# Kernel optimization log

Measured on AMD Instinct MI355X. Metric: run time of the kernel, lower is better.

The kernel has to match this reference:

```python
import jax, jax.numpy as jnp
import numpy as np
import math

B, L, D, H = 8, 1024, 1024, 16  # batch, seq, hidden_dim, num_heads
HD = D // H  # head dim = 64
CLUSTERING = True  # softmax over query axis (dim 1 of [B*H, Lq, Lk])


def setup_inputs() -> dict:
    key = jax.random.key(0)
    ks = jax.random.split(key, 12)
    s = 1.0 / math.sqrt(D)  # torch Linear default init scale-ish
    return {
        "x_q": jax.random.normal(ks[0], (B, L, D), jnp.float32),
        "x_k": jax.random.normal(ks[1], (B, L, D), jnp.float32),
        "x_v": jax.random.normal(ks[2], (B, L, D), jnp.float32),
        "mask": jnp.ones((B, L), dtype=bool),
        "Wq": jax.random.uniform(ks[3], (D, D), jnp.float32, -s, s),
        "bq": jax.random.uniform(ks[4], (D,), jnp.float32, -s, s),
        "Wk": jax.random.uniform(ks[5], (D, D), jnp.float32, -s, s),
        "bk": jax.random.uniform(ks[6], (D,), jnp.float32, -s, s),
        "Wv": jax.random.uniform(ks[7], (D, D), jnp.float32, -s, s),
        "bv": jax.random.uniform(ks[8], (D,), jnp.float32, -s, s),
        "Wo": jax.random.uniform(ks[9], (D, D), jnp.float32, -s, s),
        "bo": jax.random.uniform(ks[10], (D,), jnp.float32, -s, s),
    }


def reference(x_q, x_k, x_v, mask, Wq, bq, Wk, bk, Wv, bv, Wo, bo):
    # Projections (weights stored [in, out])
    Q = x_q @ Wq + bq  # [B, Lq, D]
    K = x_k @ Wk + bk  # [B, Lk, D]
    V = x_v @ Wv + bv  # [B, Lk, D]
    b, lq, _ = Q.shape
    lk = K.shape[1]
    # torch.cat(split(dim_split, 2), dim=0) == reshape to [B, L, H, HD] heads
    Qh = Q.reshape(b, lq, H, HD)
    Kh = K.reshape(b, lk, H, HD)
    Vh = V.reshape(b, lk, H, HD)
    # Scores scaled by sqrt(hidden_dim), NOT sqrt(head_dim) (faithful to source)
    scores = jnp.einsum("bqhd,bkhd->bhqk", Qh, Kh) / math.sqrt(D)
    # NOTE: source computes inf_mask but never applies it -> mask unused.
    if CLUSTERING:
        A = jax.nn.softmax(scores, axis=2)  # softmax over QUERY axis
    else:
        A = jax.nn.softmax(scores, axis=3)  # standard: over key axis
    # dropout ratio 0.0 -> identity
    out = jnp.einsum("bhqk,bkhd->bqhd", A, Vh).reshape(b, lq, D)
    return out @ Wo + bo
```

## Files before the change

### kernel.cpp

```cpp
#include <hip/hip_runtime.h>
#include <hip/hip_bf16.h>

#define B_ 8
#define L_ 1024
#define D_ 1024
#define H_ 16
#define HD_ 64

typedef short short8 __attribute__((ext_vector_type(8)));
typedef float floatx4 __attribute__((ext_vector_type(4)));
typedef unsigned short u16;

__device__ __forceinline__ u16 f2bf(float f) {
  union { float f; unsigned u; } v; v.f = f;
  unsigned r = v.u + 0x7fffu + ((v.u >> 16) & 1u);
  return (u16)(r >> 16);
}
__device__ __forceinline__ unsigned pk2(float a, float b) {
  union { float f; unsigned u; } x, y; x.f = a; y.f = b;
  return __builtin_amdgcn_perm(y.u + 0x8000u, x.u + 0x8000u, 0x07060302u);
}
__device__ __forceinline__ floatx4 mfma16(short8 a, short8 b, floatx4 c) {
  return __builtin_amdgcn_mfma_f32_16x16x32_bf16(a, b, c, 0, 0, 0);
}
__device__ __forceinline__ void gl2lds16(const void* g, void* l) {
  __builtin_amdgcn_global_load_lds(
      (const __attribute__((address_space(1))) void*)g,
      (__attribute__((address_space(3))) void*)l, 16, 0, 0);
}

__global__ __launch_bounds__(256) void cvtx_k(const float* __restrict__ x,
                                              u16* __restrict__ y) {
  size_t i = ((size_t)blockIdx.x * 256 + threadIdx.x) * 8;
  float4 a = *(const float4*)(x + i);
  float4 b = *(const float4*)(x + i + 4);
  uint4 u = make_uint4(pk2(a.x, a.y), pk2(a.z, a.w), pk2(b.x, b.y), pk2(b.z, b.w));
  *(uint4*)(y + i) = u;
}

__global__ __launch_bounds__(256) void cvtw_k(const float* __restrict__ W,
                                              u16* __restrict__ Wt) {
  const int kt = blockIdx.x, nt = blockIdx.y;
  __shared__ __align__(16) u16 t[64 * 72];
  const int tid = threadIdx.x;
  #pragma unroll
  for (int i = 0; i < 4; ++i) {
    int idx = i * 256 + tid;
    int r = idx >> 4, c4 = idx & 15;
    float4 v = *(const float4*)(W + (size_t)(kt * 64 + r) * 1024 + nt * 64 + c4 * 4);
    t[(c4 * 4 + 0) * 72 + r] = f2bf(v.x);
    t[(c4 * 4 + 1) * 72 + r] = f2bf(v.y);
    t[(c4 * 4 + 2) * 72 + r] = f2bf(v.z);
    t[(c4 * 4 + 3) * 72 + r] = f2bf(v.w);
  }
  __syncthreads();
  #pragma unroll
  for (int i = 0; i < 2; ++i) {
    int idx = i * 256 + tid;
    int n = idx >> 3, k8 = idx & 7;
    short8 v = *(const short8*)(&t[n * 72 + k8 * 8]);
    *(short8*)(Wt + (size_t)(nt * 64 + n) * 1024 + kt * 64 + k8 * 8) = v;
  }
}

template<int AMODE, int OUTM>
__global__ __launch_bounds__(256, 2) void gemm2_k(const void* __restrict__ Ap,
    const u16* __restrict__ Bt, const float* __restrict__ bias,
    void* __restrict__ Cp, const float* __restrict__ inv)
{
  const int nt = blockIdx.x, mt = blockIdx.y;
  const int tid = threadIdx.x, lane = tid & 63, w = tid >> 6;
  const int quad = lane >> 4, l16 = lane & 15;
  const int wm = w >> 1, wn = w & 1;
  const int m0 = mt * 128, n0 = nt * 128;

  constexpr int ABYTES = AMODE ? 8192 : 16384;
  constexpr int STG = ABYTES + 8192;
  constexpr int SBYTES = (OUTM == 2 && STG < 34816) ? 34816 : STG;
  __shared__ __align__(16) char smem[SBYTES];
  char* AsB = smem;
  char* BsB = smem + ABYTES;

  const floatx4 fz = {0.f, 0.f, 0.f, 0.f};
  floatx4 acc[4][4];
  #pragma unroll
  for (int i = 0; i < 4; ++i)
    #pragma unroll
    for (int j = 0; j < 4; ++j) acc[i][j] = fz;

  const int sw4 = (l16 & 3) ^ ((l16 >> 2) & 3);

  for (int k0 = 0; k0 < 1024; k0 += 32) {
    #pragma unroll
    for (int seg = 0; seg < 2; ++seg) {
      int cI = seg * 256 + w * 64 + lane;
      int n = cI >> 2, sl = cI & 3;
      int kc = sl ^ ((n & 3) ^ ((n >> 2) & 3));
      gl2lds16(Bt + (size_t)(n0 + n) * 1024 + k0 + kc * 8, BsB + cI * 16);
    }
    if constexpr (AMODE == 0) {
      const float* A = (const float*)Ap;
      #pragma unroll
      for (int seg = 0; seg < 4; ++seg) {
        int cI = seg * 256 + w * 64 + lane;
        int r = cI >> 3, sl = cI & 7;
        int kc = sl ^ ((r & 7) ^ ((r >> 3) & 7));
        gl2lds16(A + (size_t)(m0 + r) * 1024 + k0 + kc * 4, AsB + cI * 16);
      }
    } else {
      const u16* A = (const u16*)Ap;
      #pragma unroll
      for (int seg = 0; seg < 2; ++seg) {
        int cI = seg * 256 + w * 64 + lane;
        int r = cI >> 2, sl = cI & 3;
        int kc = sl ^ ((r & 3) ^ ((r >> 2) & 3));
        gl2lds16(A + (size_t)(m0 + r) * 1024 + k0 + kc * 8, AsB + cI * 16);
      }
    }
    __syncthreads();

    short8 af[4], bfv[4];
    #pragma unroll
    for (int mf = 0; mf < 4; ++mf) {
      int row = wm * 64 + mf * 16 + l16;
      if constexpr (AMODE == 0) {
        int s0 = (quad * 2) ^ (l16 & 7) ^ ((mf * 2 + (l16 >> 3)) & 7);
        float4 x0 = *(const float4*)(AsB + row * 128 + s0 * 16);
        float4 x1 = *(const float4*)(AsB + row * 128 + (s0 ^ 1) * 16);
        union { uint4 u; short8 s; } uu;
        uu.u = make_uint4(pk2(x0.x, x0.y), pk2(x0.z, x0.w),
                          pk2(x1.x, x1.y), pk2(x1.z, x1.w));
        af[mf] = uu.s;
      } else {
        af[mf] = *(const short8*)(AsB + row * 64 + (quad ^ sw4) * 16);
      }
    }
    #pragma unroll
    for (int nf = 0; nf < 4; ++nf) {
      int row = wn * 64 + nf * 16 + l16;
      bfv[nf] = *(const short8*)(BsB + row * 64 + (quad ^ sw4) * 16);
    }
    #pragma unroll
    for (int mf = 0; mf < 4; ++mf)
      #pragma unroll
      for (int nf = 0; nf < 4; ++nf)
        acc[mf][nf] = mfma16(af[mf], bfv[nf], acc[mf][nf]);
    __syncthreads();
  }

  float bv[4];
  #pragma unroll
  for (int nf = 0; nf < 4; ++nf) bv[nf] = bias[n0 + wn * 64 + nf * 16 + l16];

  if constexpr (OUTM == 0) {
    float* C = (float*)Cp;
    #pragma unroll
    for (int mf = 0; mf < 4; ++mf)
      #pragma unroll
      for (int nf = 0; nf < 4; ++nf) {
        int n = n0 + wn * 64 + nf * 16 + l16;
        #pragma unroll
        for (int r = 0; r < 4; ++r) {
          int m = m0 + wm * 64 + mf * 16 + quad * 4 + r;
          C[(size_t)m * 1024 + n] = acc[mf][nf][r] + bv[nf];
        }
      }
  } else if constexpr (OUTM == 1) {
    u16* C = (u16*)Cp;
    #pragma unroll
    for (int mf = 0; mf < 4; ++mf)
      #pragma unroll
      for (int nf = 0; nf < 4; ++nf) {
        int n = n0 + wn * 64 + nf * 16 + l16;
        #pragma unroll
        for (int r = 0; r < 4; ++r) {
          int m = m0 + wm * 64 + mf * 16 + quad * 4 + r;
          int bb = m >> 10, l = m & 1023, hh = n >> 6, hd = n & 63;
          C[((size_t)((bb * H_ + hh) * L_) + l) * HD_ + hd] =
              f2bf(acc[mf][nf][r] + bv[nf]);
        }
      }
  } else {
    u16* ct = (u16*)smem;
    const int bb = m0 >> 10;
    const int hrow = bb * 16 + (n0 >> 6) + wn;
    float ivv[4][4];
    #pragma unroll
    for (int mf = 0; mf < 4; ++mf)
      #pragma unroll
      for (int r = 0; r < 4; ++r)
        ivv[mf][r] = inv[(size_t)hrow * 1024 + (m0 & 1023) + wm * 64 + mf * 16 + quad * 4 + r];
    #pragma unroll
    for (int mf = 0; mf < 4; ++mf)
      #pragma unroll
      for (int nf = 0; nf < 4; ++nf)
        #pragma unroll
        for (int r = 0; r < 4; ++r) {
          float val = (acc[mf][nf][r] + bv[nf]) * ivv[mf][r];
          ct[(wn * 64 + nf * 16 + l16) * 136 + wm * 64 + mf * 16 + quad * 4 + r] = f2bf(val);
        }
    __syncthreads();
    u16* Vt = (u16*)Cp;
    #pragma unroll
    for (int i = 0; i < 8; ++i) {
      int cc = i * 256 + tid;
      int n = cc >> 4, l8 = cc & 15;
      int g = l8 >> 2, q2 = l8 & 3;
      int mloc = g * 32 + q2 * 4;
      uint2 lo = *(const uint2*)(&ct[n * 136 + mloc]);
      uint2 hi = *(const uint2*)(&ct[n * 136 + mloc + 16]);
      uint4 uv = make_uint4(lo.x, lo.y, hi.x, hi.y);
      *(uint4*)(Vt + ((size_t)bb * 1024 + n0 + n) * 1024 + (m0 & 1023) + l8 * 8) = uv;
    }
  }
}

__global__ __launch_bounds__(256, 2) void colsum2_k(const u16* __restrict__ Q,
    const u16* __restrict__ K, float* __restrict__ inv)
{
  const int ktb = blockIdx.x, h = blockIdx.y, b = blockIdx.z;
  const int tid = threadIdx.x, lane = tid & 63, w = tid >> 6;
  const int quad = lane >> 4, l16 = lane & 15;
  const size_t hb = (size_t)(b * H_ + h) * L_ * HD_;
  const u16* Qh = Q + hb;
  const u16* Kh = K + hb;
  const int kbase = ktb * 256 + w * 64;
  const floatx4 fz = {0.f, 0.f, 0.f, 0.f};
  const float cexp = 0.04508422f;

  __shared__ __align__(16) u16 qsm[8192];

  short8 kf[4][2];
  #pragma unroll
  for (int nf = 0; nf < 4; ++nf)
    #pragma unroll
    for (int ks = 0; ks < 2; ++ks)
      kf[nf][ks] = *(const short8*)(Kh + (size_t)(kbase + nf * 16 + l16) * 64 + ks * 32 + quad * 8);

  float cs[4] = {0.f, 0.f, 0.f, 0.f};
  for (int qc = 0; qc < 8; ++qc) {
    #pragma unroll
    for (int seg = 0; seg < 4; ++seg) {
      int cI = seg * 256 + w * 64 + lane;
      int row = cI >> 3, sl = cI & 7;
      gl2lds16(Qh + (size_t)(qc * 128 + row) * 64 + ((sl ^ (row & 7)) * 8), (char*)qsm + cI * 16);
    }
    __syncthreads();
    #pragma unroll
    for (int mf = 0; mf < 8; ++mf) {
      short8 qf0 = *(const short8*)(&qsm[(mf * 16 + l16) * 64 + ((quad ^ (l16 & 7)) * 8)]);
      short8 qf1 = *(const short8*)(&qsm[(mf * 16 + l16) * 64 + (((4 + quad) ^ (l16 & 7)) * 8)]);
      floatx4 sacc[4];
      #pragma unroll
      for (int nf = 0; nf < 4; ++nf) {
        floatx4 s = mfma16(qf0, kf[nf][0], fz);
        sacc[nf] = mfma16(qf1, kf[nf][1], s);
      }
      #pragma unroll
      for (int nf = 0; nf < 4; ++nf)
        #pragma unroll
        for (int r = 0; r < 4; ++r)
          cs[nf] += __builtin_amdgcn_exp2f(sacc[nf][r] * cexp);
    }
    __syncthreads();
  }
  #pragma unroll
  for (int nf = 0; nf < 4; ++nf) {
    cs[nf] += __shfl_xor(cs[nf], 16);
    cs[nf] += __shfl_xor(cs[nf], 32);
  }
  if (quad == 0) {
    #pragma unroll
    for (int nf = 0; nf < 4; ++nf)
      inv[(size_t)(b * H_ + h) * L_ + kbase + nf * 16 + l16] = 1.0f / cs[nf];
  }
}

__global__ __launch_bounds__(256, 2) void attn3_k(const u16* __restrict__ Q,
    const u16* __restrict__ K, const u16* __restrict__ Vt, u16* __restrict__ O)
{
  const int qb = blockIdx.x, h = blockIdx.y, b = blockIdx.z;
  const int tid = threadIdx.x, lane = tid & 63, w = tid >> 6;
  const int quad = lane >> 4, l16 = lane & 15;
  const size_t hb = (size_t)(b * H_ + h) * L_ * HD_;
  const u16* Qh = Q + hb;
  const u16* Kh = K + hb;
  const u16* Vh = Vt + ((size_t)b * D_ + h * HD_) * L_;
  const int q0 = qb * 256 + w * 64;
  const floatx4 fz = {0.f, 0.f, 0.f, 0.f};
  const float cexp = 0.04508422f;

  __shared__ __align__(16) u16 smem[18432];
  u16* ksb = smem;
  u16* vsb = smem + 4096;

  short8 qf[4][2];
  #pragma unroll
  for (int qs = 0; qs < 4; ++qs)
    #pragma unroll
    for (int ks = 0; ks < 2; ++ks)
      qf[qs][ks] = *(const short8*)(Qh + (size_t)(q0 + qs * 16 + l16) * 64 + ks * 32 + quad * 8);

  floatx4 oT[4][4];
  #pragma unroll
  for (int i = 0; i < 4; ++i)
    #pragma unroll
    for (int j = 0; j < 4; ++j) oT[i][j] = fz;

  for (int kc = 0; kc < 16; ++kc) {
    const int kk = kc * 64;
    #pragma unroll
    for (int seg = 0; seg < 2; ++seg) {
      int cI = seg * 256 + w * 64 + lane;
      int row = cI >> 3, sl = cI & 7;
      gl2lds16(Kh + (size_t)(kk + row) * 64 + ((sl ^ (row & 7)) * 8), (char*)ksb + cI * 16);
    }
    #pragma unroll
    for (int seg = 0; seg < 2; ++seg) {
      int cI = seg * 256 + w * 64 + lane;
      int row = cI >> 3, sl = cI & 7;
      gl2lds16(Vh + (size_t)row * L_ + kk + ((sl ^ (row & 7)) * 8), (char*)vsb + cI * 16);
    }
    __syncthreads();

    short8 pt[2][4];
    #pragma unroll
    for (int p = 0; p < 2; ++p) {
      short8 ka0[2], ka1[2];
      #pragma unroll
      for (int ks = 0; ks < 2; ++ks) {
        ka0[ks] = *(const short8*)(&ksb[((2 * p) * 16 + l16) * 64 + (((ks * 4 + quad) ^ (l16 & 7)) * 8)]);
        ka1[ks] = *(const short8*)(&ksb[((2 * p + 1) * 16 + l16) * 64 + (((ks * 4 + quad) ^ (l16 & 7)) * 8)]);
      }
      #pragma unroll
      for (int qs = 0; qs < 4; ++qs) {
        floatx4 s0 = mfma16(ka0[0], qf[qs][0], fz);
        s0 = mfma16(ka0[1], qf[qs][1], s0);
        floatx4 s1 = mfma16(ka1[0], qf[qs][0], fz);
        s1 = mfma16(ka1[1], qf[qs][1], s1);
        float e0 = __builtin_amdgcn_exp2f(s0[0] * cexp);
        float e1 = __builtin_amdgcn_exp2f(s0[1] * cexp);
        float e2 = __builtin_amdgcn_exp2f(s0[2] * cexp);
        float e3 = __builtin_amdgcn_exp2f(s0[3] * cexp);
        float f0 = __builtin_amdgcn_exp2f(s1[0] * cexp);
        float f1 = __builtin_amdgcn_exp2f(s1[1] * cexp);
        float f2 = __builtin_amdgcn_exp2f(s1[2] * cexp);
        float f3 = __builtin_amdgcn_exp2f(s1[3] * cexp);
        union { uint4 u; short8 s; } pu;
        pu.u = make_uint4(pk2(e0, e1), pk2(e2, e3), pk2(f0, f1), pk2(f2, f3));
        pt[p][qs] = pu.s;
      }
    }
    #pragma unroll
    for (int p = 0; p < 2; ++p) {
      #pragma unroll
      for (int ds = 0; ds < 4; ++ds) {
        short8 va = *(const short8*)(&vsb[(ds * 16 + l16) * 64 + (((p * 4 + quad) ^ (l16 & 7)) * 8)]);
        #pragma unroll
        for (int qs = 0; qs < 4; ++qs)
          oT[ds][qs] = mfma16(va, pt[p][qs], oT[ds][qs]);
      }
    }
    __syncthreads();
  }

  u16* ot = smem + w * 4608;
  #pragma unroll
  for (int ds = 0; ds < 4; ++ds)
    #pragma unroll
    for (int qs = 0; qs < 4; ++qs)
      #pragma unroll
      for (int r = 0; r < 4; ++r)
        ot[(qs * 16 + l16) * 72 + ds * 16 + quad * 4 + r] = f2bf(oT[ds][qs][r]);
  __syncthreads();
  #pragma unroll
  for (int i = 0; i < 8; ++i) {
    int cc = i * 64 + lane;
    int ql = cc >> 3, d8 = cc & 7;
    short8 v = *(const short8*)(&ot[ql * 72 + d8 * 8]);
    *(short8*)(O + ((size_t)b * L_ + q0 + ql) * D_ + h * HD_ + d8 * 8) = v;
  }
}

extern "C" void kernel_launch(void* const* d_in, const int* in_sizes, int n_in,
                              void* d_out, int out_size, void* d_ws, size_t ws_size,
                              hipStream_t stream) {
  const float* xq = (const float*)d_in[0];
  const float* xk = (const float*)d_in[1];
  const float* xv = (const float*)d_in[2];
  const float* Wq = (const float*)d_in[4];
  const float* bq = (const float*)d_in[5];
  const float* Wk = (const float*)d_in[6];
  const float* bk = (const float*)d_in[7];
  const float* Wv = (const float*)d_in[8];
  const float* bv = (const float*)d_in[9];
  const float* Wo = (const float*)d_in[10];
  const float* bo = (const float*)d_in[11];

  char* ws = (char*)d_ws;
  const size_t MB16 = 16u << 20;
  u16* Xbf  = (u16*)(ws);
  u16* Vtb  = (u16*)(ws);
  u16* Qb   = (u16*)(ws + MB16);
  u16* WT2  = (u16*)(ws + MB16);
  u16* Kb   = (u16*)(ws + 2 * MB16);
  u16* WT   = (u16*)(ws + 3 * MB16);
  float* invb = (float*)(ws + 3 * MB16 + (2u << 20));
  u16* Ob   = (u16*)(ws + 3 * MB16);

  dim3 blk(256);
  dim3 gw(16, 16);
  dim3 gg(8, 64);

  cvtx_k<<<4096, blk, 0, stream>>>(xq, Xbf);
  cvtw_k<<<gw, blk, 0, stream>>>(Wq, WT);
  gemm2_k<1, 1><<<gg, blk, 0, stream>>>(Xbf, WT, bq, Qb, nullptr);

  cvtx_k<<<4096, blk, 0, stream>>>(xk, Xbf);
  cvtw_k<<<gw, blk, 0, stream>>>(Wk, WT);
  gemm2_k<1, 1><<<gg, blk, 0, stream>>>(Xbf, WT, bk, Kb, nullptr);

  colsum2_k<<<dim3(4, 16, 8), blk, 0, stream>>>(Qb, Kb, invb);

  cvtw_k<<<gw, blk, 0, stream>>>(Wv, WT);
  gemm2_k<0, 2><<<gg, blk, 0, stream>>>(xv, WT, bv, Vtb, invb);

  attn3_k<<<dim3(4, 16, 8), blk, 0, stream>>>(Qb, Kb, Vtb, Ob);

  cvtw_k<<<gw, blk, 0, stream>>>(Wo, WT2);
  gemm2_k<1, 0><<<gg, blk, 0, stream>>>(Ob, WT2, bo, (float*)d_out, nullptr);
}
```

Measured before the change: 373.4 us.

## Double K-step tiles in GEMM and attention, batch conversion kernels into fewer launches

```diff
diff --git a/kernel.cpp b/kernel.cpp
--- a/kernel.cpp
+++ b/kernel.cpp
@@ -29,8 +29,11 @@
       (__attribute__((address_space(3))) void*)l, 16, 0, 0);
 }
 
-__global__ __launch_bounds__(256) void cvtx_k(const float* __restrict__ x,
-                                              u16* __restrict__ y) {
+__global__ __launch_bounds__(256) void cvtx3_k(const float* __restrict__ x0,
+    const float* __restrict__ x1, const float* __restrict__ x2,
+    u16* __restrict__ y0, u16* __restrict__ y1, u16* __restrict__ y2) {
+  const float* x = blockIdx.y == 0 ? x0 : (blockIdx.y == 1 ? x1 : x2);
+  u16* y = blockIdx.y == 0 ? y0 : (blockIdx.y == 1 ? y1 : y2);
   size_t i = ((size_t)blockIdx.x * 256 + threadIdx.x) * 8;
   float4 a = *(const float4*)(x + i);
   float4 b = *(const float4*)(x + i + 4);
@@ -38,8 +41,14 @@
   *(uint4*)(y + i) = u;
 }
 
-__global__ __launch_bounds__(256) void cvtw_k(const float* __restrict__ W,
-                                              u16* __restrict__ Wt) {
+__global__ __launch_bounds__(256) void cvtw4_k(
+    const float* __restrict__ W0, const float* __restrict__ W1,
+    const float* __restrict__ W2, const float* __restrict__ W3,
+    u16* __restrict__ T0, u16* __restrict__ T1,
+    u16* __restrict__ T2, u16* __restrict__ T3) {
+  const int z = blockIdx.z;
+  const float* W = z == 0 ? W0 : (z == 1 ? W1 : (z == 2 ? W2 : W3));
+  u16* Wt = z == 0 ? T0 : (z == 1 ? T1 : (z == 2 ? T2 : T3));
   const int kt = blockIdx.x, nt = blockIdx.y;
   __shared__ __align__(16) u16 t[64 * 72];
   const int tid = threadIdx.x;
@@ -74,8 +83,8 @@
   const int wm = w >> 1, wn = w & 1;
   const int m0 = mt * 128, n0 = nt * 128;
 
-  constexpr int ABYTES = AMODE ? 8192 : 16384;
-  constexpr int STG = ABYTES + 8192;
+  constexpr int ABYTES = AMODE ? 16384 : 32768;
+  constexpr int STG = ABYTES + 16384;
   constexpr int SBYTES = (OUTM == 2 && STG < 34816) ? 34816 : STG;
   __shared__ __align__(16) char smem[SBYTES];
   char* AsB = smem;
@@ -88,63 +97,64 @@
     #pragma unroll
     for (int j = 0; j < 4; ++j) acc[i][j] = fz;
 
-  const int sw4 = (l16 & 3) ^ ((l16 >> 2) & 3);
-
-  for (int k0 = 0; k0 < 1024; k0 += 32) {
-    #pragma unroll
-    for (int seg = 0; seg < 2; ++seg) {
+  for (int k0 = 0; k0 < 1024; k0 += 64) {
+    #pragma unroll
+    for (int seg = 0; seg < 4; ++seg) {
       int cI = seg * 256 + w * 64 + lane;
-      int n = cI >> 2, sl = cI & 3;
-      int kc = sl ^ ((n & 3) ^ ((n >> 2) & 3));
-      gl2lds16(Bt + (size_t)(n0 + n) * 1024 + k0 + kc * 8, BsB + cI * 16);
+      int r = cI >> 3, sl = cI & 7;
+      int kc = sl ^ (r & 7);
+      gl2lds16(Bt + (size_t)(n0 + r) * 1024 + k0 + kc * 8, BsB + cI * 16);
     }
     if constexpr (AMODE == 0) {
       const float* A = (const float*)Ap;
+      #pragma unroll
+      for (int seg = 0; seg < 8; ++seg) {
+        int cI = seg * 256 + w * 64 + lane;
+        int r = cI >> 4, sl = cI & 15;
+        int kc = sl ^ (r & 15);
+        gl2lds16(A + (size_t)(m0 + r) * 1024 + k0 + kc * 4, AsB + cI * 16);
+      }
+    } else {
+      const u16* A = (const u16*)Ap;
       #pragma unroll
       for (int seg = 0; seg < 4; ++seg) {
         int cI = seg * 256 + w * 64 + lane;
         int r = cI >> 3, sl = cI & 7;
-        int kc = sl ^ ((r & 7) ^ ((r >> 3) & 7));
-        gl2lds16(A + (size_t)(m0 + r) * 1024 + k0 + kc * 4, AsB + cI * 16);
-      }
-    } else {
-      const u16* A = (const u16*)Ap;
-      #pragma unroll
-      for (int seg = 0; seg < 2; ++seg) {
-        int cI = seg * 256 + w * 64 + lane;
-        int r = cI >> 2, sl = cI & 3;
-        int kc = sl ^ ((r & 3) ^ ((r >> 2) & 3));
+        int kc = sl ^ (r & 7);
         gl2lds16(A + (size_t)(m0 + r) * 1024 + k0 + kc * 8, AsB + cI * 16);
       }
     }
     __syncthreads();
 
-    short8 af[4], bfv[4];
-    #pragma unroll
-    for (int mf = 0; mf < 4; ++mf) {
-      int row = wm * 64 + mf * 16 + l16;
-      if constexpr (AMODE == 0) {
-        int s0 = (quad * 2) ^ (l16 & 7) ^ ((mf * 2 + (l16 >> 3)) & 7);
-        float4 x0 = *(const float4*)(AsB + row * 128 + s0 * 16);
-        float4 x1 = *(const float4*)(AsB + row * 128 + (s0 ^ 1) * 16);
-        union { uint4 u; short8 s; } uu;
-        uu.u = make_uint4(pk2(x0.x, x0.y), pk2(x0.z, x0.w),
-                          pk2(x1.x, x1.y), pk2(x1.z, x1.w));
-        af[mf] = uu.s;
-      } else {
-        af[mf] = *(const short8*)(AsB + row * 64 + (quad ^ sw4) * 16);
-      }
-    }
-    #pragma unroll
-    for (int nf = 0; nf < 4; ++nf) {
-      int row = wn * 64 + nf * 16 + l16;
-      bfv[nf] = *(const short8*)(BsB + row * 64 + (quad ^ sw4) * 16);
-    }
-    #pragma unroll
-    for (int mf = 0; mf < 4; ++mf)
-      #pragma unroll
-      for (int nf = 0; nf < 4; ++nf)
-        acc[mf][nf] = mfma16(af[mf], bfv[nf], acc[mf][nf]);
+    #pragma unroll
+    for (int ks = 0; ks < 2; ++ks) {
+      short8 af[4], bfv[4];
+      #pragma unroll
+      for (int mf = 0; mf < 4; ++mf) {
+        int row = wm * 64 + mf * 16 + l16;
+        if constexpr (AMODE == 0) {
+          int L0 = ks * 8 + quad * 2;
+          float4 x0 = *(const float4*)(AsB + row * 256 + ((L0) ^ l16) * 16);
+          float4 x1 = *(const float4*)(AsB + row * 256 + ((L0 + 1) ^ l16) * 16);
+          union { uint4 u; short8 s; } uu;
+          uu.u = make_uint4(pk2(x0.x, x0.y), pk2(x0.z, x0.w),
+                            pk2(x1.x, x1.y), pk2(x1.z, x1.w));
+          af[mf] = uu.s;
+        } else {
+          af[mf] = *(const short8*)(AsB + row * 128 + (((ks * 4 + quad) ^ (l16 & 7)) * 16));
+        }
+      }
+      #pragma unroll
+      for (int nf = 0; nf < 4; ++nf) {
+        int row = wn * 64 + nf * 16 + l16;
+        bfv[nf] = *(const short8*)(BsB + row * 128 + (((ks * 4 + quad) ^ (l16 & 7)) * 16));
+      }
+      #pragma unroll
+      for (int mf = 0; mf < 4; ++mf)
+        #pragma unroll
+        for (int nf = 0; nf < 4; ++nf)
+          acc[mf][nf] = mfma16(af[mf], bfv[nf], acc[mf][nf]);
+    }
     __syncthreads();
   }
 
@@ -190,6 +200,7 @@
       #pragma unroll
       for (int r = 0; r < 4; ++r)
         ivv[mf][r] = inv[(size_t)hrow * 1024 + (m0 & 1023) + wm * 64 + mf * 16 + quad * 4 + r];
+    __syncthreads();
     #pragma unroll
     for (int mf = 0; mf < 4; ++mf)
       #pragma unroll
@@ -228,7 +239,7 @@
   const floatx4 fz = {0.f, 0.f, 0.f, 0.f};
   const float cexp = 0.04508422f;
 
-  __shared__ __align__(16) u16 qsm[8192];
+  __shared__ __align__(16) u16 qsm[16384];
 
   short8 kf[4][2];
   #pragma unroll
@@ -238,16 +249,16 @@
       kf[nf][ks] = *(const short8*)(Kh + (size_t)(kbase + nf * 16 + l16) * 64 + ks * 32 + quad * 8);
 
   float cs[4] = {0.f, 0.f, 0.f, 0.f};
-  for (int qc = 0; qc < 8; ++qc) {
-    #pragma unroll
-    for (int seg = 0; seg < 4; ++seg) {
+  for (int qc = 0; qc < 4; ++qc) {
+    #pragma unroll
+    for (int seg = 0; seg < 8; ++seg) {
       int cI = seg * 256 + w * 64 + lane;
       int row = cI >> 3, sl = cI & 7;
-      gl2lds16(Qh + (size_t)(qc * 128 + row) * 64 + ((sl ^ (row & 7)) * 8), (char*)qsm + cI * 16);
-    }
-    __syncthreads();
-    #pragma unroll
-    for (int mf = 0; mf < 8; ++mf) {
+      gl2lds16(Qh + (size_t)(qc * 256 + row) * 64 + ((sl ^ (row & 7)) * 8), (char*)qsm + cI * 16);
+    }
+    __syncthreads();
+    #pragma unroll
+    for (int mf = 0; mf < 16; ++mf) {
       short8 qf0 = *(const short8*)(&qsm[(mf * 16 + l16) * 64 + ((quad ^ (l16 & 7)) * 8)]);
       short8 qf1 = *(const short8*)(&qsm[(mf * 16 + l16) * 64 + (((4 + quad) ^ (l16 & 7)) * 8)]);
       floatx4 sacc[4];
@@ -292,7 +303,7 @@
 
   __shared__ __align__(16) u16 smem[18432];
   u16* ksb = smem;
-  u16* vsb = smem + 4096;
+  u16* vsb = smem + 8192;
 
   short8 qf[4][2];
   #pragma unroll
@@ -307,31 +318,31 @@
     #pragma unroll
     for (int j = 0; j < 4; ++j) oT[i][j] = fz;
 
-  for (int kc = 0; kc < 16; ++kc) {
-    const int kk = kc * 64;
-    #pragma unroll
-    for (int seg = 0; seg < 2; ++seg) {
+  for (int kc = 0; kc < 8; ++kc) {
+    const int kk = kc * 128;
+    #pragma unroll
+    for (int seg = 0; seg < 4; ++seg) {
       int cI = seg * 256 + w * 64 + lane;
       int row = cI >> 3, sl = cI & 7;
       gl2lds16(Kh + (size_t)(kk + row) * 64 + ((sl ^ (row & 7)) * 8), (char*)ksb + cI * 16);
     }
     #pragma unroll
-    for (int seg = 0; seg < 2; ++seg) {
+    for (int seg = 0; seg < 4; ++seg) {
       int cI = seg * 256 + w * 64 + lane;
-      int row = cI >> 3, sl = cI & 7;
-      gl2lds16(Vh + (size_t)row * L_ + kk + ((sl ^ (row & 7)) * 8), (char*)vsb + cI * 16);
-    }
-    __syncthreads();
-
-    short8 pt[2][4];
-    #pragma unroll
-    for (int p = 0; p < 2; ++p) {
+      int row = cI >> 4, sl = cI & 15;
+      gl2lds16(Vh + (size_t)row * L_ + kk + ((sl ^ (row & 15)) * 8), (char*)vsb + cI * 16);
+    }
+    __syncthreads();
+
+    #pragma unroll
+    for (int p = 0; p < 4; ++p) {
       short8 ka0[2], ka1[2];
       #pragma unroll
       for (int ks = 0; ks < 2; ++ks) {
-        ka0[ks] = *(const short8*)(&ksb[((2 * p) * 16 + l16) * 64 + (((ks * 4 + quad) ^ (l16 & 7)) * 8)]);
-        ka1[ks] = *(const short8*)(&ksb[((2 * p + 1) * 16 + l16) * 64 + (((ks * 4 + quad) ^ (l16 & 7)) * 8)]);
-      }
+        ka0[ks] = *(const short8*)((char*)ksb + (p * 32 + l16) * 128 + (((ks * 4 + quad) ^ (l16 & 7)) * 16));
+        ka1[ks] = *(const short8*)((char*)ksb + (p * 32 + 16 + l16) * 128 + (((ks * 4 + quad) ^ (l16 & 7)) * 16));
+      }
+      short8 pt[4];
       #pragma unroll
       for (int qs = 0; qs < 4; ++qs) {
         floatx4 s0 = mfma16(ka0[0], qf[qs][0], fz);
@@ -348,17 +359,14 @@
         float f3 = __builtin_amdgcn_exp2f(s1[3] * cexp);
         union { uint4 u; short8 s; } pu;
         pu.u = make_uint4(pk2(e0, e1), pk2(e2, e3), pk2(f0, f1), pk2(f2, f3));
-        pt[p][qs] = pu.s;
-      }
-    }
-    #pragma unroll
-    for (int p = 0; p < 2; ++p) {
+        pt[qs] = pu.s;
+      }
       #pragma unroll
       for (int ds = 0; ds < 4; ++ds) {
-        short8 va = *(const short8*)(&vsb[(ds * 16 + l16) * 64 + (((p * 4 + quad) ^ (l16 & 7)) * 8)]);
+        short8 va = *(const short8*)((char*)vsb + (ds * 16 + l16) * 256 + (((p * 4 + quad) ^ l16) * 16));
         #pragma unroll
         for (int qs = 0; qs < 4; ++qs)
-          oT[ds][qs] = mfma16(va, pt[p][qs], oT[ds][qs]);
+          oT[ds][qs] = mfma16(va, pt[qs], oT[ds][qs]);
       }
     }
     __syncthreads();
@@ -398,35 +406,54 @@
   const float* bo = (const float*)d_in[11];
 
   char* ws = (char*)d_ws;
-  const size_t MB16 = 16u << 20;
-  u16* Xbf  = (u16*)(ws);
-  u16* Vtb  = (u16*)(ws);
-  u16* Qb   = (u16*)(ws + MB16);
-  u16* WT2  = (u16*)(ws + MB16);
-  u16* Kb   = (u16*)(ws + 2 * MB16);
-  u16* WT   = (u16*)(ws + 3 * MB16);
-  float* invb = (float*)(ws + 3 * MB16 + (2u << 20));
-  u16* Ob   = (u16*)(ws + 3 * MB16);
-
+  const size_t MB = 1u << 20;
   dim3 blk(256);
-  dim3 gw(16, 16);
   dim3 gg(8, 64);
 
-  cvtx_k<<<4096, blk, 0, stream>>>(xq, Xbf);
-  cvtw_k<<<gw, blk, 0, stream>>>(Wq, WT);
-  gemm2_k<1, 1><<<gg, blk, 0, stream>>>(Xbf, WT, bq, Qb, nullptr);
-
-  cvtx_k<<<4096, blk, 0, stream>>>(xk, Xbf);
-  cvtw_k<<<gw, blk, 0, stream>>>(Wk, WT);
-  gemm2_k<1, 1><<<gg, blk, 0, stream>>>(Xbf, WT, bk, Kb, nullptr);
-
-  colsum2_k<<<dim3(4, 16, 8), blk, 0, stream>>>(Qb, Kb, invb);
-
-  cvtw_k<<<gw, blk, 0, stream>>>(Wv, WT);
-  gemm2_k<0, 2><<<gg, blk, 0, stream>>>(xv, WT, bv, Vtb, invb);
-
-  attn3_k<<<dim3(4, 16, 8), blk, 0, stream>>>(Qb, Kb, Vtb, Ob);
-
-  cvtw_k<<<gw, blk, 0, stream>>>(Wo, WT2);
-  gemm2_k<1, 0><<<gg, blk, 0, stream>>>(Ob, WT2, bo, (float*)d_out, nullptr);
-}
+  if (ws_size >= 90 * MB) {
+    u16* xqb = (u16*)(ws);
+    u16* xkb = (u16*)(ws + 16 * MB);
+    u16* xvb = (u16*)(ws + 32 * MB);
+    u16* WTq = (u16*)(ws + 48 * MB);
+    u16* WTk = (u16*)(ws + 50 * MB);
+    u16* WTv = (u16*)(ws + 52 * MB);
+    u16* WTo = (u16*)(ws + 54 * MB);
+    float* invb = (float*)(ws + 56 * MB);
+    u16* Qb = (u16*)(ws + 57 * MB);
+    u16* Kb = (u16*)(ws + 73 * MB);
+    u16* Vtb = (u16*)(ws);
+    u16* Ob = (u16*)(ws + 16 * MB);
+
+    cvtx3_k<<<dim3(4096, 3), blk, 0, stream>>>(xq, xk, xv, xqb, xkb, xvb);
+    cvtw4_k<<<dim3(16, 16, 4), blk, 0, stream>>>(Wq, Wk, Wv, Wo, WTq, WTk, WTv, WTo);
+    gemm2_k<1, 1><<<gg, blk, 0, stream>>>(xqb, WTq, bq, Qb, nullptr);
+    gemm2_k<1, 1><<<gg, blk, 0, stream>>>(xkb, WTk, bk, Kb, nullptr);
+    colsum2_k<<<dim3(4, 16, 8), blk, 0, stream>>>(Qb, Kb, invb);
+    gemm2_k<1, 2><<<gg, blk, 0, stream>>>(xvb, WTv, bv, Vtb, invb);
+    attn3_k<<<dim3(4, 16, 8), blk, 0, stream>>>(Qb, Kb, Vtb, Ob);
+    gemm2_k<1, 0><<<gg, blk, 0, stream>>>(Ob, WTo, bo, (float*)d_out, nullptr);
+  } else {
+    const size_t MB16 = 16u << 20;
+    u16* Xbf  = (u16*)(ws);
+    u16* Vtb  = (u16*)(ws);
+    u16* Qb   = (u16*)(ws + MB16);
+    u16* WT2  = (u16*)(ws + MB16);
+    u16* Kb   = (u16*)(ws + 2 * MB16);
+    u16* WT   = (u16*)(ws + 3 * MB16);
+    float* invb = (float*)(ws + 3 * MB16 + (2u << 20));
+    u16* Ob   = (u16*)(ws + 3 * MB16);
+
+    cvtx3_k<<<dim3(4096, 1), blk, 0, stream>>>(xq, xq, xq, Xbf, Xbf, Xbf);
+    cvtw4_k<<<dim3(16, 16, 1), blk, 0, stream>>>(Wq, Wq, Wq, Wq, WT, WT, WT, WT);
+    gemm2_k<1, 1><<<gg, blk, 0, stream>>>(Xbf, WT, bq, Qb, nullptr);
+    cvtx3_k<<<dim3(4096, 1), blk, 0, stream>>>(xk, xk, xk, Xbf, Xbf, Xbf);
+    cvtw4_k<<<dim3(16, 16, 1), blk, 0, stream>>>(Wk, Wk, Wk, Wk, WT, WT, WT, WT);
+    gemm2_k<1, 1><<<gg, blk, 0, stream>>>(Xbf, WT, bk, Kb, nullptr);
+    colsum2_k<<<dim3(4, 16, 8), blk, 0, stream>>>(Qb, Kb, invb);
+    cvtw4_k<<<dim3(16, 16, 1), blk, 0, stream>>>(Wv, Wv, Wv, Wv, WT, WT, WT, WT);
+    gemm2_k<0, 2><<<gg, blk, 0, stream>>>(xv, WT, bv, Vtb, invb);
+    attn3_k<<<dim3(4, 16, 8), blk, 0, stream>>>(Qb, Kb, Vtb, Ob);
+    cvtw4_k<<<dim3(16, 16, 1), blk, 0, stream>>>(Wo, Wo, Wo, Wo, WT2, WT2, WT2, WT2);
+    gemm2_k<1, 0><<<gg, blk, 0, stream>>>(Ob, WT2, bo, (float*)d_out, nullptr);
+  }
+}
```

Result: faster. 335.9 us (-10.0%).
